# Optimization experiments

Measured on AMD Instinct MI355X. Metric: run time of the kernel, lower is better.

Reference implementation:

```python
import jax, jax.numpy as jnp
import numpy as np

NUM_CLUSTERS = 512


def setup_inputs() -> dict:
    key = jax.random.key(0)
    k1, k2 = jax.random.split(key)
    N, F, K = 131072, 64, NUM_CLUSTERS
    z_e = jax.random.normal(k1, (N, F), dtype=jnp.float32)
    # torch init: uniform(-1/K, 1/K) for embedding weight [F, K]
    W = jax.random.uniform(k2, (F, K), dtype=jnp.float32, minval=-1.0 / K, maxval=1.0 / K)
    return {"z_e": z_e, "W": W}


def reference(z_e, W):
    # squared-distance matrix [N, K] via expansion: ||z||^2 - 2 z.W + ||w||^2
    distances = (
        jnp.sum(z_e * z_e, axis=1, keepdims=True)
        - 2.0 * (z_e @ W)
        + jnp.sum(W * W, axis=0, keepdims=True)
    )
    encoding_idx = jnp.argmin(distances, axis=-1)  # [N]
    encodings = jax.nn.one_hot(encoding_idx, NUM_CLUSTERS, dtype=z_e.dtype)  # [N, K]
    z_q = jnp.take(W, encoding_idx, axis=1).T  # gather == encodings @ W.T, [N, F]
    diff = (jax.lax.stop_gradient(z_q) - z_e) ** 2
    z_q = z_e + jax.lax.stop_gradient(z_q - z_e)  # straight-through
    return z_q, encoding_idx[:, None], encodings, diff
```

## Files before the change

### kernel.cpp

```cpp
#include <hip/hip_runtime.h>

#define K_CLUSTERS 512
#define FDIM 64
#define RPB 512
#define RT 8
#define NTILES 4
#define WSTRIDE 17

typedef float vf4 __attribute__((ext_vector_type(4)));

__global__ __launch_bounds__(64) void vq_prep(const float* __restrict__ W,
                                              float* __restrict__ Wt,
                                              float* __restrict__ wsq) {
    int k = blockIdx.x;
    int f = threadIdx.x;
    float w = W[f * K_CLUSTERS + k];
    Wt[k * FDIM + f] = w;
    float s = w * w;
#pragma unroll
    for (int off = 32; off > 0; off >>= 1) s += __shfl_xor(s, off, 64);
    if (f == 0) wsq[k] = s;
}

__global__ __launch_bounds__(1024)
__attribute__((amdgpu_waves_per_eu(4, 4)))
void vq_fused(const float* __restrict__ z,
              const float* __restrict__ W,
              const float* __restrict__ Wt,
              const float* __restrict__ wsq,
              float* __restrict__ out_zq,
              float* __restrict__ out_idx,
              float* __restrict__ enc,
              float* __restrict__ out_diff) {
    __shared__ vf4 sW4[K_CLUSTERS * WSTRIDE];

    const int tid = threadIdx.x;
    const int w = __builtin_amdgcn_readfirstlane(tid) >> 6;
    const int l = tid & 63;

    {
        float* sWf = (float*)sW4;
        const vf4* Wg4 = (const vf4*)W;
#pragma unroll
        for (int it = 0; it < 8; it++) {
            int u4 = it * 1024 + tid;
            vf4 v = Wg4[u4];
            int u = u4 << 2;
            int f = u >> 9;
            int c0 = u & 511;
            int f4 = f >> 2, m = f & 3;
#pragma unroll
            for (int e = 0; e < 4; e++) {
                int c = c0 + e;
                sWf[c * (4 * WSTRIDE) + (f4 << 2) + m] = v[e];
            }
        }
    }
    __syncthreads();

    const int rowW = blockIdx.x * RPB + w * (RT * NTILES);
    const vf4* zg4 = (const vf4*)z;

#pragma unroll 1
    for (int t = 0; t < NTILES; t++) {
        const int row0 = rowW + t * RT;

        float srow;
        {
            const float* zr = z + (size_t)(row0 + (l >> 3)) * FDIM;
            const int j = l & 7;
            float rj;
            {
#pragma clang fp contract(off)
                rj = zr[j] * zr[j];
#pragma unroll
                for (int b = 8; b < 64; b += 8) rj += zr[b + j] * zr[b + j];
            }
            float s01 = rj + __shfl_xor(rj, 1, 64);
            float s03 = s01 + __shfl_xor(s01, 2, 64);
            srow = s03 + __shfl_xor(s03, 4, 64);
        }
        float sA[RT];
#pragma unroll
        for (int r = 0; r < RT; r++) sA[r] = __shfl(srow, r << 3, 64);

        float bd[RT];
        int bk[RT];
#pragma unroll
        for (int r = 0; r < RT; r++) { bd[r] = INFINITY; bk[r] = 0; }

        const vf4* zt = zg4 + (size_t)row0 * 16;

#pragma unroll 1
        for (int pass = 0; pass < 2; pass++) {
            const int cBase = (pass << 8) + l;
            float q0 = wsq[cBase];
            float q1 = wsq[cBase + 64];
            float q2 = wsq[cBase + 128];
            float q3 = wsq[cBase + 192];
            float acc[RT][4];
#pragma unroll
            for (int r = 0; r < RT; r++)
#pragma unroll
                for (int jj = 0; jj < 4; jj++) acc[r][jj] = 0.0f;
            const vf4* wB = sW4 + cBase * WSTRIDE;
#pragma unroll 2
            for (int f4 = 0; f4 < 16; f4++) {
                vf4 wv0 = wB[f4];
                vf4 wv1 = wB[64 * WSTRIDE + f4];
                vf4 wv2 = wB[128 * WSTRIDE + f4];
                vf4 wv3 = wB[192 * WSTRIDE + f4];
#pragma unroll
                for (int r = 0; r < RT; r++) {
                    vf4 zb = zt[(r << 4) + f4];
                    float a0 = acc[r][0], a1 = acc[r][1], a2 = acc[r][2], a3 = acc[r][3];
                    a0 = fmaf(zb.x, wv0.x, a0); a1 = fmaf(zb.x, wv1.x, a1);
                    a2 = fmaf(zb.x, wv2.x, a2); a3 = fmaf(zb.x, wv3.x, a3);
                    a0 = fmaf(zb.y, wv0.y, a0); a1 = fmaf(zb.y, wv1.y, a1);
                    a2 = fmaf(zb.y, wv2.y, a2); a3 = fmaf(zb.y, wv3.y, a3);
                    a0 = fmaf(zb.z, wv0.z, a0); a1 = fmaf(zb.z, wv1.z, a1);
                    a2 = fmaf(zb.z, wv2.z, a2); a3 = fmaf(zb.z, wv3.z, a3);
                    a0 = fmaf(zb.w, wv0.w, a0); a1 = fmaf(zb.w, wv1.w, a1);
                    a2 = fmaf(zb.w, wv2.w, a2); a3 = fmaf(zb.w, wv3.w, a3);
                    acc[r][0] = a0; acc[r][1] = a1; acc[r][2] = a2; acc[r][3] = a3;
                }
            }
#pragma unroll
            for (int r = 0; r < RT; r++) {
                float d0 = fmaf(-2.0f, acc[r][0], sA[r]) + q0;
                float d1 = fmaf(-2.0f, acc[r][1], sA[r]) + q1;
                float d2 = fmaf(-2.0f, acc[r][2], sA[r]) + q2;
                float d3 = fmaf(-2.0f, acc[r][3], sA[r]) + q3;
                if (d0 < bd[r] || (d0 == bd[r] && cBase < bk[r])) { bd[r] = d0; bk[r] = cBase; }
                if (d1 < bd[r] || (d1 == bd[r] && cBase + 64 < bk[r])) { bd[r] = d1; bk[r] = cBase + 64; }
                if (d2 < bd[r] || (d2 == bd[r] && cBase + 128 < bk[r])) { bd[r] = d2; bk[r] = cBase + 128; }
                if (d3 < bd[r] || (d3 == bd[r] && cBase + 192 < bk[r])) { bd[r] = d3; bk[r] = cBase + 192; }
            }
        }

#pragma unroll
        for (int off = 1; off < 64; off <<= 1) {
#pragma unroll
            for (int r = 0; r < RT; r++) {
                float od = __shfl_xor(bd[r], off, 64);
                int ok = __shfl_xor(bk[r], off, 64);
                if (od < bd[r] || (od == bd[r] && ok < bk[r])) { bd[r] = od; bk[r] = ok; }
            }
        }

        if (l == 0) {
#pragma unroll
            for (int r = 0; r < RT; r++) out_idx[row0 + r] = (float)bk[r];
        }

#pragma unroll
        for (int h = 0; h < 2; h++) {
            const int rsel = l >> 4;
            int kk = bk[4 * h + 0];
            if (rsel == 1) kk = bk[4 * h + 1];
            if (rsel == 2) kk = bk[4 * h + 2];
            if (rsel == 3) kk = bk[4 * h + 3];
            vf4 zvv = zt[(h << 6) + l];
            vf4 wvv = ((const vf4*)Wt)[((size_t)kk << 4) + (l & 15)];
            vf4 zq, df;
            {
#pragma clang fp contract(off)
                vf4 d1 = wvv - zvv;
                zq = zvv + d1;
                df = d1 * d1;
            }
            ((vf4*)out_zq)[(size_t)row0 * 16 + (h << 6) + l] = zq;
            ((vf4*)out_diff)[(size_t)row0 * 16 + (h << 6) + l] = df;
        }

        {
            vf4* enc4 = (vf4*)enc + (size_t)row0 * 128;
#pragma unroll
            for (int jj = 0; jj < 16; jj++) {
                const int row = jj >> 1;
                int kk = bk[row];
                int c = kk - ((l + ((jj & 1) << 6)) << 2);
                vf4 v;
                v.x = (c == 0) ? 1.0f : 0.0f;
                v.y = (c == 1) ? 1.0f : 0.0f;
                v.z = (c == 2) ? 1.0f : 0.0f;
                v.w = (c == 3) ? 1.0f : 0.0f;
                enc4[(jj << 6) + l] = v;
            }
        }
    }
}

extern "C" void kernel_launch(void* const* d_in, const int* in_sizes, int n_in,
                              void* d_out, int out_size, void* d_ws, size_t ws_size,
                              hipStream_t stream) {
    const float* z = (const float*)d_in[0];
    const float* W = (const float*)d_in[1];
    int N = in_sizes[0] / FDIM;

    float* out = (float*)d_out;
    float* out_zq = out;
    float* out_idx = out_zq + (size_t)N * FDIM;
    float* enc = out_idx + N;
    float* out_diff = enc + (size_t)N * K_CLUSTERS;

    float* Wt = (float*)d_ws;
    float* wsq = Wt + K_CLUSTERS * FDIM;

    vq_prep<<<K_CLUSTERS, 64, 0, stream>>>(W, Wt, wsq);
    vq_fused<<<N / RPB, 1024, 0, stream>>>(z, W, Wt, wsq, out_zq, out_idx, enc, out_diff);
}
```

Baseline: 447.4 us.

## Stage codebook in two LDS halves to double occupancy with smaller row tiles

The codebook now goes into shared memory in two 256-cluster stages instead of all 512 at once, which halves the LDS footprint. The per-row running argmin is carried across stages in shared arrays. Rows per block drop to 256 and rows per tile to 4, and the waves-per-EU target rises from 4 to 8, so more blocks can be resident to hide memory latency. In exchange, each z row's norm and dot products are reloaded once per stage, two extra barriers are added per stage, and each tile is loaded with less data reuse.

```diff
diff --git a/kernel.cpp b/kernel.cpp
--- a/kernel.cpp
+++ b/kernel.cpp
@@ -2,9 +2,10 @@
 
 #define K_CLUSTERS 512
 #define FDIM 64
-#define RPB 512
-#define RT 8
-#define NTILES 4
+#define RPB 256
+#define RT 4
+#define NT 4
+#define CSTAGE 256
 #define WSTRIDE 17
 
 typedef float vf4 __attribute__((ext_vector_type(4)));
@@ -23,7 +24,7 @@
 }
 
 __global__ __launch_bounds__(1024)
-__attribute__((amdgpu_waves_per_eu(4, 4)))
+__attribute__((amdgpu_waves_per_eu(8, 8)))
 void vq_fused(const float* __restrict__ z,
               const float* __restrict__ W,
               const float* __restrict__ Wt,
@@ -32,79 +33,77 @@
               float* __restrict__ out_idx,
               float* __restrict__ enc,
               float* __restrict__ out_diff) {
-    __shared__ vf4 sW4[K_CLUSTERS * WSTRIDE];
+    __shared__ vf4 sW4[CSTAGE * WSTRIDE];
+    __shared__ float sd[RPB];
+    __shared__ int sk[RPB];
 
     const int tid = threadIdx.x;
     const int w = __builtin_amdgcn_readfirstlane(tid) >> 6;
     const int l = tid & 63;
 
-    {
-        float* sWf = (float*)sW4;
-        const vf4* Wg4 = (const vf4*)W;
-#pragma unroll
-        for (int it = 0; it < 8; it++) {
-            int u4 = it * 1024 + tid;
-            vf4 v = Wg4[u4];
-            int u = u4 << 2;
-            int f = u >> 9;
-            int c0 = u & 511;
-            int f4 = f >> 2, m = f & 3;
-#pragma unroll
-            for (int e = 0; e < 4; e++) {
-                int c = c0 + e;
-                sWf[c * (4 * WSTRIDE) + (f4 << 2) + m] = v[e];
+    if (tid < RPB) { sd[tid] = INFINITY; sk[tid] = 0; }
+
+    const int rowW = blockIdx.x * RPB + (w << 4);
+    const vf4* zg4 = (const vf4*)z;
+    const vf4* wB = sW4 + l * WSTRIDE;
+
+#pragma unroll 1
+    for (int p = 0; p < 2; p++) {
+        __syncthreads();
+        {
+            float* sWf = (float*)sW4;
+            const vf4* Wg4 = (const vf4*)W;
+#pragma unroll
+            for (int it = 0; it < 4; it++) {
+                int u = (it << 10) + tid;
+                int f = u & 63;
+                int col4 = u >> 6;
+                vf4 v = Wg4[f * 128 + (p << 6) + col4];
+#pragma unroll
+                for (int e = 0; e < 4; e++) {
+                    int cl = (col4 << 2) + e;
+                    sWf[cl * (4 * WSTRIDE) + f] = v[e];
+                }
             }
         }
-    }
-    __syncthreads();
-
-    const int rowW = blockIdx.x * RPB + w * (RT * NTILES);
-    const vf4* zg4 = (const vf4*)z;
+        __syncthreads();
+
+        const int cOff = p << 8;
 
 #pragma unroll 1
-    for (int t = 0; t < NTILES; t++) {
-        const int row0 = rowW + t * RT;
-
-        float srow;
-        {
-            const float* zr = z + (size_t)(row0 + (l >> 3)) * FDIM;
-            const int j = l & 7;
-            float rj;
+        for (int t = 0; t < NT; t++) {
+            const int row0 = rowW + (t << 2);
+            const int lrow0 = (w << 4) + (t << 2);
+
+            float srow;
             {
+                const float* zr = z + (size_t)(row0 + ((l >> 3) & 3)) * FDIM;
+                const int j = l & 7;
+                float rj;
+                {
 #pragma clang fp contract(off)
-                rj = zr[j] * zr[j];
-#pragma unroll
-                for (int b = 8; b < 64; b += 8) rj += zr[b + j] * zr[b + j];
-            }
-            float s01 = rj + __shfl_xor(rj, 1, 64);
-            float s03 = s01 + __shfl_xor(s01, 2, 64);
-            srow = s03 + __shfl_xor(s03, 4, 64);
-        }
-        float sA[RT];
-#pragma unroll
-        for (int r = 0; r < RT; r++) sA[r] = __shfl(srow, r << 3, 64);
-
-        float bd[RT];
-        int bk[RT];
-#pragma unroll
-        for (int r = 0; r < RT; r++) { bd[r] = INFINITY; bk[r] = 0; }
-
-        const vf4* zt = zg4 + (size_t)row0 * 16;
+                    rj = zr[j] * zr[j];
+#pragma unroll
+                    for (int b = 8; b < 64; b += 8) rj += zr[b + j] * zr[b + j];
+                }
+                float s01 = rj + __shfl_xor(rj, 1, 64);
+                float s03 = s01 + __shfl_xor(s01, 2, 64);
+                srow = s03 + __shfl_xor(s03, 4, 64);
+            }
+            const float sA0 = __shfl(srow, 0, 64);
+            const float sA1 = __shfl(srow, 8, 64);
+            const float sA2 = __shfl(srow, 16, 64);
+            const float sA3 = __shfl(srow, 24, 64);
+
+            const vf4* zt = zg4 + (size_t)row0 * 16;
+
+            float acc[RT][4];
+#pragma unroll
+            for (int r = 0; r < RT; r++)
+#pragma unroll
+                for (int j = 0; j < 4; j++) acc[r][j] = 0.0f;
 
 #pragma unroll 1
-        for (int pass = 0; pass < 2; pass++) {
-            const int cBase = (pass << 8) + l;
-            float q0 = wsq[cBase];
-            float q1 = wsq[cBase + 64];
-            float q2 = wsq[cBase + 128];
-            float q3 = wsq[cBase + 192];
-            float acc[RT][4];
-#pragma unroll
-            for (int r = 0; r < RT; r++)
-#pragma unroll
-                for (int jj = 0; jj < 4; jj++) acc[r][jj] = 0.0f;
-            const vf4* wB = sW4 + cBase * WSTRIDE;
-#pragma unroll 2
             for (int f4 = 0; f4 < 16; f4++) {
                 vf4 wv0 = wB[f4];
                 vf4 wv1 = wB[64 * WSTRIDE + f4];
@@ -125,67 +124,84 @@
                     acc[r][0] = a0; acc[r][1] = a1; acc[r][2] = a2; acc[r][3] = a3;
                 }
             }
-#pragma unroll
-            for (int r = 0; r < RT; r++) {
-                float d0 = fmaf(-2.0f, acc[r][0], sA[r]) + q0;
-                float d1 = fmaf(-2.0f, acc[r][1], sA[r]) + q1;
-                float d2 = fmaf(-2.0f, acc[r][2], sA[r]) + q2;
-                float d3 = fmaf(-2.0f, acc[r][3], sA[r]) + q3;
-                if (d0 < bd[r] || (d0 == bd[r] && cBase < bk[r])) { bd[r] = d0; bk[r] = cBase; }
-                if (d1 < bd[r] || (d1 == bd[r] && cBase + 64 < bk[r])) { bd[r] = d1; bk[r] = cBase + 64; }
-                if (d2 < bd[r] || (d2 == bd[r] && cBase + 128 < bk[r])) { bd[r] = d2; bk[r] = cBase + 128; }
-                if (d3 < bd[r] || (d3 == bd[r] && cBase + 192 < bk[r])) { bd[r] = d3; bk[r] = cBase + 192; }
-            }
-        }
-
-#pragma unroll
-        for (int off = 1; off < 64; off <<= 1) {
-#pragma unroll
-            for (int r = 0; r < RT; r++) {
-                float od = __shfl_xor(bd[r], off, 64);
-                int ok = __shfl_xor(bk[r], off, 64);
-                if (od < bd[r] || (od == bd[r] && ok < bk[r])) { bd[r] = od; bk[r] = ok; }
-            }
-        }
-
-        if (l == 0) {
-#pragma unroll
-            for (int r = 0; r < RT; r++) out_idx[row0 + r] = (float)bk[r];
-        }
-
-#pragma unroll
-        for (int h = 0; h < 2; h++) {
-            const int rsel = l >> 4;
-            int kk = bk[4 * h + 0];
-            if (rsel == 1) kk = bk[4 * h + 1];
-            if (rsel == 2) kk = bk[4 * h + 2];
-            if (rsel == 3) kk = bk[4 * h + 3];
-            vf4 zvv = zt[(h << 6) + l];
-            vf4 wvv = ((const vf4*)Wt)[((size_t)kk << 4) + (l & 15)];
-            vf4 zq, df;
-            {
+
+            float bd[RT];
+            int bk[RT];
+            bd[0] = sd[lrow0 + 0]; bk[0] = sk[lrow0 + 0];
+            bd[1] = sd[lrow0 + 1]; bk[1] = sk[lrow0 + 1];
+            bd[2] = sd[lrow0 + 2]; bk[2] = sk[lrow0 + 2];
+            bd[3] = sd[lrow0 + 3]; bk[3] = sk[lrow0 + 3];
+#pragma unroll
+            for (int j = 0; j < 4; j++) {
+                const int c = cOff + (j << 6) + l;
+                const float q = wsq[c];
+                float d0 = fmaf(-2.0f, acc[0][j], sA0) + q;
+                float d1 = fmaf(-2.0f, acc[1][j], sA1) + q;
+                float d2 = fmaf(-2.0f, acc[2][j], sA2) + q;
+                float d3 = fmaf(-2.0f, acc[3][j], sA3) + q;
+                if (d0 < bd[0] || (d0 == bd[0] && c < bk[0])) { bd[0] = d0; bk[0] = c; }
+                if (d1 < bd[1] || (d1 == bd[1] && c < bk[1])) { bd[1] = d1; bk[1] = c; }
+                if (d2 < bd[2] || (d2 == bd[2] && c < bk[2])) { bd[2] = d2; bk[2] = c; }
+                if (d3 < bd[3] || (d3 == bd[3] && c < bk[3])) { bd[3] = d3; bk[3] = c; }
+            }
+
+#pragma unroll
+            for (int off = 1; off < 64; off <<= 1) {
+#pragma unroll
+                for (int r = 0; r < RT; r++) {
+                    float od = __shfl_xor(bd[r], off, 64);
+                    int ok = __shfl_xor(bk[r], off, 64);
+                    if (od < bd[r] || (od == bd[r] && ok < bk[r])) { bd[r] = od; bk[r] = ok; }
+                }
+            }
+
+            if (p == 0) {
+                if (l == 0) {
+                    sd[lrow0 + 0] = bd[0]; sk[lrow0 + 0] = bk[0];
+                    sd[lrow0 + 1] = bd[1]; sk[lrow0 + 1] = bk[1];
+                    sd[lrow0 + 2] = bd[2]; sk[lrow0 + 2] = bk[2];
+                    sd[lrow0 + 3] = bd[3]; sk[lrow0 + 3] = bk[3];
+                }
+            } else {
+                if (l == 0) {
+                    out_idx[row0 + 0] = (float)bk[0];
+                    out_idx[row0 + 1] = (float)bk[1];
+                    out_idx[row0 + 2] = (float)bk[2];
+                    out_idx[row0 + 3] = (float)bk[3];
+                }
+                {
+                    const int rsel = l >> 4;
+                    int kk = bk[0];
+                    if (rsel == 1) kk = bk[1];
+                    if (rsel == 2) kk = bk[2];
+                    if (rsel == 3) kk = bk[3];
+                    vf4 zvv = zt[l];
+                    vf4 wvv = ((const vf4*)Wt)[((size_t)kk << 4) + (l & 15)];
+                    vf4 zq, df;
+                    {
 #pragma clang fp contract(off)
-                vf4 d1 = wvv - zvv;
-                zq = zvv + d1;
-                df = d1 * d1;
-            }
-            ((vf4*)out_zq)[(size_t)row0 * 16 + (h << 6) + l] = zq;
-            ((vf4*)out_diff)[(size_t)row0 * 16 + (h << 6) + l] = df;
-        }
-
-        {
-            vf4* enc4 = (vf4*)enc + (size_t)row0 * 128;
-#pragma unroll
-            for (int jj = 0; jj < 16; jj++) {
-                const int row = jj >> 1;
-                int kk = bk[row];
-                int c = kk - ((l + ((jj & 1) << 6)) << 2);
-                vf4 v;
-                v.x = (c == 0) ? 1.0f : 0.0f;
-                v.y = (c == 1) ? 1.0f : 0.0f;
-                v.z = (c == 2) ? 1.0f : 0.0f;
-                v.w = (c == 3) ? 1.0f : 0.0f;
-                enc4[(jj << 6) + l] = v;
+                        vf4 d1 = wvv - zvv;
+                        zq = zvv + d1;
+                        df = d1 * d1;
+                    }
+                    ((vf4*)out_zq)[(size_t)row0 * 16 + l] = zq;
+                    ((vf4*)out_diff)[(size_t)row0 * 16 + l] = df;
+                }
+                {
+                    vf4* enc4 = (vf4*)enc + (size_t)row0 * 128;
+#pragma unroll
+                    for (int jj = 0; jj < 8; jj++) {
+                        const int row = jj >> 1;
+                        int kk = bk[row];
+                        int c = kk - ((l + ((jj & 1) << 6)) << 2);
+                        vf4 v;
+                        v.x = (c == 0) ? 1.0f : 0.0f;
+                        v.y = (c == 1) ? 1.0f : 0.0f;
+                        v.z = (c == 2) ? 1.0f : 0.0f;
+                        v.w = (c == 3) ? 1.0f : 0.0f;
+                        enc4[(jj << 6) + l] = v;
+                    }
+                }
             }
         }
     }
```

Result: no change. 454.7 us (+1.6%).

## Hold z rows in registers, broadcast with readlane, prefetch next tile and W

Applied to the files above, without the earlier changes.

Each lane now keeps one element of each of the tile's 8 z rows in a VGPR and broadcasts values with v_readlane inside the distance FMA loop, replacing the per-iteration uniform global loads of z. The next tile's z rows are prefetched into registers during the current tile. The shared-memory codebook loads are software-pipelined one f4 step ahead. The aim is to take global z-load latency out of the inner loop, at the cost of many readlane instructions, extra VGPR pressure and possible readlane hazard stalls.

```diff
diff --git a/kernel.cpp b/kernel.cpp
--- a/kernel.cpp
+++ b/kernel.cpp
@@ -61,9 +61,21 @@
     const int rowW = blockIdx.x * RPB + w * (RT * NTILES);
     const vf4* zg4 = (const vf4*)z;
 
+    float zreg[RT];
+#pragma unroll
+    for (int r = 0; r < RT; r++) zreg[r] = z[(size_t)(rowW + r) * FDIM + l];
+
 #pragma unroll 1
     for (int t = 0; t < NTILES; t++) {
         const int row0 = rowW + t * RT;
+
+        float zregN[RT];
+        {
+            const int rows_next = (t < NTILES - 1) ? row0 + RT : row0;
+#pragma unroll
+            for (int r = 0; r < RT; r++)
+                zregN[r] = z[(size_t)(rows_next + r) * FDIM + l];
+        }
 
         float srow;
         {
@@ -89,42 +101,56 @@
 #pragma unroll
         for (int r = 0; r < RT; r++) { bd[r] = INFINITY; bk[r] = 0; }
 
-        const vf4* zt = zg4 + (size_t)row0 * 16;
-
 #pragma unroll 1
         for (int pass = 0; pass < 2; pass++) {
             const int cBase = (pass << 8) + l;
-            float q0 = wsq[cBase];
-            float q1 = wsq[cBase + 64];
-            float q2 = wsq[cBase + 128];
-            float q3 = wsq[cBase + 192];
             float acc[RT][4];
 #pragma unroll
             for (int r = 0; r < RT; r++)
 #pragma unroll
                 for (int jj = 0; jj < 4; jj++) acc[r][jj] = 0.0f;
-            const vf4* wB = sW4 + cBase * WSTRIDE;
+
+            const vf4* wP = sW4 + (size_t)cBase * WSTRIDE;
+            vf4 w0 = wP[0];
+            vf4 w1 = wP[64 * WSTRIDE];
+            vf4 w2 = wP[128 * WSTRIDE];
+            vf4 w3 = wP[192 * WSTRIDE];
+
 #pragma unroll 2
             for (int f4 = 0; f4 < 16; f4++) {
-                vf4 wv0 = wB[f4];
-                vf4 wv1 = wB[64 * WSTRIDE + f4];
-                vf4 wv2 = wB[128 * WSTRIDE + f4];
-                vf4 wv3 = wB[192 * WSTRIDE + f4];
+                const int fp = (f4 + 1) & 15;
+                vf4 n0 = wP[fp];
+                vf4 n1 = wP[64 * WSTRIDE + fp];
+                vf4 n2 = wP[128 * WSTRIDE + fp];
+                vf4 n3 = wP[192 * WSTRIDE + fp];
 #pragma unroll
                 for (int r = 0; r < RT; r++) {
-                    vf4 zb = zt[(r << 4) + f4];
+                    float zx = __int_as_float(__builtin_amdgcn_readlane(
+                        __float_as_int(zreg[r]), (f4 << 2) + 0));
+                    float zy = __int_as_float(__builtin_amdgcn_readlane(
+                        __float_as_int(zreg[r]), (f4 << 2) + 1));
+                    float zz = __int_as_float(__builtin_amdgcn_readlane(
+                        __float_as_int(zreg[r]), (f4 << 2) + 2));
+                    float zw = __int_as_float(__builtin_amdgcn_readlane(
+                        __float_as_int(zreg[r]), (f4 << 2) + 3));
                     float a0 = acc[r][0], a1 = acc[r][1], a2 = acc[r][2], a3 = acc[r][3];
-                    a0 = fmaf(zb.x, wv0.x, a0); a1 = fmaf(zb.x, wv1.x, a1);
-                    a2 = fmaf(zb.x, wv2.x, a2); a3 = fmaf(zb.x, wv3.x, a3);
-                    a0 = fmaf(zb.y, wv0.y, a0); a1 = fmaf(zb.y, wv1.y, a1);
-                    a2 = fmaf(zb.y, wv2.y, a2); a3 = fmaf(zb.y, wv3.y, a3);
-                    a0 = fmaf(zb.z, wv0.z, a0); a1 = fmaf(zb.z, wv1.z, a1);
-                    a2 = fmaf(zb.z, wv2.z, a2); a3 = fmaf(zb.z, wv3.z, a3);
-                    a0 = fmaf(zb.w, wv0.w, a0); a1 = fmaf(zb.w, wv1.w, a1);
-                    a2 = fmaf(zb.w, wv2.w, a2); a3 = fmaf(zb.w, wv3.w, a3);
+                    a0 = fmaf(zx, w0.x, a0); a1 = fmaf(zx, w1.x, a1);
+                    a2 = fmaf(zx, w2.x, a2); a3 = fmaf(zx, w3.x, a3);
+                    a0 = fmaf(zy, w0.y, a0); a1 = fmaf(zy, w1.y, a1);
+                    a2 = fmaf(zy, w2.y, a2); a3 = fmaf(zy, w3.y, a3);
+                    a0 = fmaf(zz, w0.z, a0); a1 = fmaf(zz, w1.z, a1);
+                    a2 = fmaf(zz, w2.z, a2); a3 = fmaf(zz, w3.z, a3);
+                    a0 = fmaf(zw, w0.w, a0); a1 = fmaf(zw, w1.w, a1);
+                    a2 = fmaf(zw, w2.w, a2); a3 = fmaf(zw, w3.w, a3);
                     acc[r][0] = a0; acc[r][1] = a1; acc[r][2] = a2; acc[r][3] = a3;
                 }
-            }
+                w0 = n0; w1 = n1; w2 = n2; w3 = n3;
+            }
+
+            const float q0 = wsq[cBase];
+            const float q1 = wsq[cBase + 64];
+            const float q2 = wsq[cBase + 128];
+            const float q3 = wsq[cBase + 192];
 #pragma unroll
             for (int r = 0; r < RT; r++) {
                 float d0 = fmaf(-2.0f, acc[r][0], sA[r]) + q0;
@@ -153,6 +179,7 @@
             for (int r = 0; r < RT; r++) out_idx[row0 + r] = (float)bk[r];
         }
 
+        const vf4* ztv = zg4 + (size_t)row0 * 16;
 #pragma unroll
         for (int h = 0; h < 2; h++) {
             const int rsel = l >> 4;
@@ -160,7 +187,7 @@
             if (rsel == 1) kk = bk[4 * h + 1];
             if (rsel == 2) kk = bk[4 * h + 2];
             if (rsel == 3) kk = bk[4 * h + 3];
-            vf4 zvv = zt[(h << 6) + l];
+            vf4 zvv = ztv[(h << 6) + l];
             vf4 wvv = ((const vf4*)Wt)[((size_t)kk << 4) + (l & 15)];
             vf4 zq, df;
             {
@@ -188,6 +215,9 @@
                 enc4[(jj << 6) + l] = v;
             }
         }
+
+#pragma unroll
+        for (int r = 0; r < RT; r++) zreg[r] = zregN[r];
     }
 }
 
```

Result: slower. 498.7 us (+11.5%).
